# Optimization experiments

Measured on AMD Instinct MI355X. Metric: run time of the kernel, lower is better.

The kernel has to match this reference:

```python
import jax, jax.numpy as jnp
import numpy as np

S, I, H, O = 8192, 1024, 1024, 1024


def setup_inputs() -> dict:
    key = jax.random.key(0)
    ks = jax.random.split(key, 7)
    s = 1.0 / np.sqrt(H).astype(np.float32)  # PyTorch LSTM/Linear init scale
    u = lambda k, shape: jax.random.uniform(k, shape, jnp.float32, -s, s)
    return {
        "x": jax.random.normal(ks[0], (S, I), jnp.float32),
        "W_ih": u(ks[1], (4 * H, I)),   # gate order: i, f, g, o (PyTorch)
        "W_hh": u(ks[2], (4 * H, H)),
        "b_ih": u(ks[3], (4 * H,)),
        "b_hh": u(ks[4], (4 * H,)),
        "W_out": u(ks[5], (O, H)),
        "b_out": u(ks[6], (O,)),
    }


def _lstm_forward(x, W_ih, W_hh, b_ih, b_hh, W_out, b_out):
    h_dim = W_hh.shape[1]
    # Precompute input projections for all timesteps in one GEMM: [S, 4H]
    x_proj = x @ W_ih.T + (b_ih + b_hh)

    def step(carry, xp_t):
        h, c = carry                       # [H], [H]
        gates = xp_t + h @ W_hh.T          # [4H]
        i, f, g, o = jnp.split(gates, 4)
        i = jax.nn.sigmoid(i)
        f = jax.nn.sigmoid(f)
        g = jnp.tanh(g)
        o = jax.nn.sigmoid(o)
        c = f * c + i * g
        h = o * jnp.tanh(c)
        return (h, c), h

    init = (jnp.zeros((h_dim,), x.dtype), jnp.zeros((h_dim,), x.dtype))
    _, hs = jax.lax.scan(step, init, x_proj)   # hs: [S, H]
    logits = hs @ W_out.T + b_out              # [S, O]
    return jax.nn.log_softmax(logits, axis=1)


def reference(x, W_ih, W_hh, b_ih, b_hh, W_out, b_out):
    return _lstm_forward(x, W_ih, W_hh, b_ih, b_hh, W_out, b_out)
```

## Files before the change

kernel.cpp:

```cpp
#include <hip/hip_runtime.h>


using u16 = unsigned short;
using u32 = unsigned int;
using u64 = unsigned long long;

typedef short  short8  __attribute__((ext_vector_type(8)));
typedef float  floatx4 __attribute__((ext_vector_type(4)));
typedef u32    uintx4  __attribute__((ext_vector_type(4)));

#define S_LEN 8192
#define NPROD 64

__device__ __forceinline__ u16 f2bf(float f) {
    u32 u = __float_as_uint(f);
    u += 0x7FFFu + ((u >> 16) & 1u);
    return (u16)(u >> 16);
}

__device__ __forceinline__ floatx4 mfma16(short8 a, short8 b, floatx4 c) {
    return __builtin_amdgcn_mfma_f32_16x16x32_bf16(a, b, c, 0, 0, 0);
}


__global__ void cvt_f32_bf16(const float* __restrict__ src, u16* __restrict__ dst, int n) {
    for (int i = blockIdx.x * blockDim.x + threadIdx.x; i < n; i += gridDim.x * blockDim.x)
        dst[i] = f2bf(src[i]);
}

__global__ void bias_comb_k(const float* __restrict__ a, const float* __restrict__ b,
                            float* __restrict__ o) {
    int i = blockIdx.x * blockDim.x + threadIdx.x;
    if (i < 4096) o[i] = a[i] + b[i];
}

__global__ void init_hbuf(u64* __restrict__ hbuf) {
    hbuf[blockIdx.x * 256 + threadIdx.x] = 0ull;
}


__global__ __launch_bounds__(256) void gemm_bt(const u16* __restrict__ A,
                                               const u16* __restrict__ B,
                                               const float* __restrict__ bias,
                                               float* __restrict__ C,
                                               int M, int N, int K) {
    const int tid = threadIdx.x;
    const int l = tid & 63, w = tid >> 6;
    const int m0 = blockIdx.x * 128 + (w >> 1) * 64;
    const int n0 = blockIdx.y * 64 + (w & 1) * 32;
    const int lr = l & 15, lk = (l >> 4) * 8;

    floatx4 acc[4][2];
#pragma unroll
    for (int i = 0; i < 4; i++)
#pragma unroll
        for (int j = 0; j < 2; j++) acc[i][j] = floatx4{0.f, 0.f, 0.f, 0.f};

    const u16* Ap = A + (size_t)(m0 + lr) * K + lk;
    const u16* Bp = B + (size_t)(n0 + lr) * K + lk;

    for (int k0 = 0; k0 < K; k0 += 32) {
        short8 a0 = *(const short8*)(Ap + k0);
        short8 a1 = *(const short8*)(Ap + (size_t)16 * K + k0);
        short8 a2 = *(const short8*)(Ap + (size_t)32 * K + k0);
        short8 a3 = *(const short8*)(Ap + (size_t)48 * K + k0);
        short8 b0 = *(const short8*)(Bp + k0);
        short8 b1 = *(const short8*)(Bp + (size_t)16 * K + k0);
        acc[0][0] = mfma16(a0, b0, acc[0][0]); acc[0][1] = mfma16(a0, b1, acc[0][1]);
        acc[1][0] = mfma16(a1, b0, acc[1][0]); acc[1][1] = mfma16(a1, b1, acc[1][1]);
        acc[2][0] = mfma16(a2, b0, acc[2][0]); acc[2][1] = mfma16(a2, b1, acc[2][1]);
        acc[3][0] = mfma16(a3, b0, acc[3][0]); acc[3][1] = mfma16(a3, b1, acc[3][1]);
    }

    const int rr = (l >> 4) * 4;
#pragma unroll
    for (int j = 0; j < 2; j++) {
        const int n = n0 + j * 16 + lr;
        const float bv = bias[n];
#pragma unroll
        for (int i = 0; i < 4; i++) {
            const int m = m0 + i * 16 + rr;
#pragma unroll
            for (int r = 0; r < 4; r++)
                C[(size_t)(m + r) * N + n] = acc[i][j][r] + bv;
        }
    }
}


__device__ __forceinline__ float sig_f(float x) {
    return __builtin_amdgcn_rcpf(1.f + __expf(-x));
}
__device__ __forceinline__ float tanh_f(float x) {
    return 1.f - 2.f * __builtin_amdgcn_rcpf(1.f + __expf(2.f * x));
}

__global__ __launch_bounds__(512, 2) void lstm_rec(const u16* __restrict__ Whhb,
                                                   const float* __restrict__ xp,
                                                   u64* __restrict__ hbuf,
                                                   u32* __restrict__ hs) {
    const int p = blockIdx.x;
    const int tid = threadIdx.x;
    const int l = tid & 63, w = tid >> 6;
    const int g = w & 3;
    const int kh = w >> 2;

    __shared__ u32 h_lds[512];
    __shared__ float dots[128];
    __shared__ float xp_lds[2][64];

    short8 afr[16];
    {
        const u16* wr = Whhb + (size_t)(g * 1024 + p * 16 + (l & 15)) * 1024
                       + kh * 512 + ((l >> 4) * 8);
#pragma unroll
        for (int kb = 0; kb < 16; ++kb) afr[kb] = *(const short8*)(wr + kb * 32);
    }
    h_lds[tid] = 0u;

    float c_state = 0.f;
    const float* xprow = xp + (size_t)(l >> 4) * 1024 + p * 16 + (l & 15);
    if (w == 5) xp_lds[0][l] = xprow[0];
    __syncthreads();

    const int bofs = (l >> 4) * 4;
    const u32* hb_base = &h_lds[kh * 256 + bofs];
    const int pi = (w - 1) * 64 + l;

    for (int t = 0; t < S_LEN; ++t) {
        float xc = 0.f;

        if (w == 0) {
            xc = xp_lds[t & 1][l];
        } else if (w == 5) {
            int tn = (t + 1 < S_LEN) ? t + 1 : S_LEN - 1;
            xp_lds[(t + 1) & 1][l] = xprow[(size_t)tn * 4096];
        } else if (w <= 4 && t > 0) {
            u64* src0 = hbuf + (size_t)(t & 1) * 512 + 2 * pi;
            const u32 want = (u32)t;
            uintx4 q;
            bool got = false;
            for (int it = 0; it < 4096 && !got; ++it) {
                asm volatile("global_load_dwordx4 %0, %1, off sc0 sc1\n\t"
                             "s_waitcnt vmcnt(0)"
                             : "=&v"(q) : "v"(src0) : "memory");
                got = (q.y == want) && (q.w == want);
            }
            while (!got) {
                u64 a = __hip_atomic_load(src0, __ATOMIC_RELAXED,
                                          __HIP_MEMORY_SCOPE_AGENT);
                u64 b = __hip_atomic_load(src0 + 1, __ATOMIC_RELAXED,
                                          __HIP_MEMORY_SCOPE_AGENT);
                if ((u32)(a >> 32) == want && (u32)(b >> 32) == want) {
                    q.x = (u32)a; q.z = (u32)b; got = true;
                }
            }
            h_lds[2 * pi]     = q.x;
            h_lds[2 * pi + 1] = q.z;
        }
        __syncthreads();

        floatx4 ac0 = floatx4{0,0,0,0}, ac1 = floatx4{0,0,0,0};
        floatx4 ac2 = floatx4{0,0,0,0}, ac3 = floatx4{0,0,0,0};
#pragma unroll
        for (int kb = 0; kb < 16; kb += 4) {
            uintx4 b0 = *(const uintx4*)(hb_base + (kb + 0) * 16);
            uintx4 b1 = *(const uintx4*)(hb_base + (kb + 1) * 16);
            uintx4 b2 = *(const uintx4*)(hb_base + (kb + 2) * 16);
            uintx4 b3 = *(const uintx4*)(hb_base + (kb + 3) * 16);
            ac0 = mfma16(afr[kb + 0], __builtin_bit_cast(short8, b0), ac0);
            ac1 = mfma16(afr[kb + 1], __builtin_bit_cast(short8, b1), ac1);
            ac2 = mfma16(afr[kb + 2], __builtin_bit_cast(short8, b2), ac2);
            ac3 = mfma16(afr[kb + 3], __builtin_bit_cast(short8, b3), ac3);
        }
        floatx4 acs = (ac0 + ac1) + (ac2 + ac3);
        if ((l & 15) == 0) {
            const int q = l >> 4;
#pragma unroll
            for (int r = 0; r < 4; ++r) dots[kh * 64 + g * 16 + q * 4 + r] = acs[r];
        }
        __syncthreads();

        if (w == 0) {
            float a = dots[l] + dots[64 + l] + xc;
            float act = ((l >> 4) == 2) ? tanh_f(a) : sig_f(a);
            const int jj = l & 15;
            float fi = __shfl(act, jj);
            float ff = __shfl(act, 16 + jj);
            float fg = __shfl(act, 32 + jj);
            float fo = __shfl(act, 48 + jj);
            if (l < 16) {
                c_state = ff * c_state + fi * fg;
                float h = fo * tanh_f(c_state);
                u16 hb16 = f2bf(h);
                u32 other = (u32)__shfl_down((int)hb16, 1);
                if ((l & 1) == 0) {
                    u32 pk = (u32)hb16 | (other << 16);
                    int pidx = p * 8 + (l >> 1);
                    u64 tv = ((u64)(u32)(t + 1) << 32) | (u64)pk;
                    __hip_atomic_store(&hbuf[(size_t)((t + 1) & 1) * 512 + pidx], tv,
                                       __ATOMIC_RELAXED, __HIP_MEMORY_SCOPE_AGENT);
                    hs[(size_t)t * 512 + pidx] = pk;
                }
            }
        }
    }
}


__global__ __launch_bounds__(256) void lsm_k(float* __restrict__ C) {
    const int tid = threadIdx.x;
    float* p = C + (size_t)blockIdx.x * 1024;
    float v0 = p[tid], v1 = p[tid + 256], v2 = p[tid + 512], v3 = p[tid + 768];
    float mx = fmaxf(fmaxf(v0, v1), fmaxf(v2, v3));
#pragma unroll
    for (int o = 1; o < 64; o <<= 1) mx = fmaxf(mx, __shfl_xor(mx, o));
    __shared__ float red[4];
    const int w = tid >> 6, l = tid & 63;
    if (l == 0) red[w] = mx;
    __syncthreads();
    mx = fmaxf(fmaxf(red[0], red[1]), fmaxf(red[2], red[3]));
    float s = __expf(v0 - mx) + __expf(v1 - mx) + __expf(v2 - mx) + __expf(v3 - mx);
#pragma unroll
    for (int o = 1; o < 64; o <<= 1) s += __shfl_xor(s, o);
    __syncthreads();
    if (l == 0) red[w] = s;
    __syncthreads();
    s = red[0] + red[1] + red[2] + red[3];
    float ls = __logf(s) + mx;
    p[tid] = v0 - ls; p[tid + 256] = v1 - ls; p[tid + 512] = v2 - ls; p[tid + 768] = v3 - ls;
}


extern "C" void kernel_launch(void* const* d_in, const int* in_sizes, int n_in,
                              void* d_out, int out_size, void* d_ws, size_t ws_size,
                              hipStream_t stream) {
    const float* x     = (const float*)d_in[0];
    const float* W_ih  = (const float*)d_in[1];
    const float* W_hh  = (const float*)d_in[2];
    const float* b_ih  = (const float*)d_in[3];
    const float* b_hh  = (const float*)d_in[4];
    const float* W_out = (const float*)d_in[5];
    const float* b_out = (const float*)d_in[6];

    char* ws = (char*)d_ws;
    u16*   xb    = (u16*)(ws + 0);
    u16*   Wihb  = (u16*)(ws + 16777216);
    u16*   Whhb  = (u16*)(ws + 25165824);
    u16*   Woutb = (u16*)(ws + 33554432);
    float* biasc = (float*)(ws + 35651584);
    u64*   hbuf  = (u64*)(ws + 35667968);
    u32*   hs    = (u32*)(ws + 35676160);
    float* xp    = (float*)(ws + 52453376);

    init_hbuf<<<4, 256, 0, stream>>>(hbuf);
    cvt_f32_bf16<<<2048, 256, 0, stream>>>(x, xb, 8192 * 1024);
    cvt_f32_bf16<<<1024, 256, 0, stream>>>(W_ih, Wihb, 4096 * 1024);
    cvt_f32_bf16<<<1024, 256, 0, stream>>>(W_hh, Whhb, 4096 * 1024);
    cvt_f32_bf16<<<256, 256, 0, stream>>>(W_out, Woutb, 1024 * 1024);
    bias_comb_k<<<16, 256, 0, stream>>>(b_ih, b_hh, biasc);

    gemm_bt<<<dim3(64, 64), 256, 0, stream>>>(xb, Wihb, biasc, xp, 8192, 4096, 1024);

    lstm_rec<<<NPROD, 512, 0, stream>>>(Whhb, xp, hbuf, hs);

    gemm_bt<<<dim3(64, 16), 256, 0, stream>>>((const u16*)hs, Woutb, b_out, (float*)d_out,
                                              8192, 1024, 1024);

    lsm_k<<<8192, 256, 0, stream>>>((float*)d_out);
}
```

Measured before the change: 13.23 ms.

## Halve recurrent producer blocks, each computing 32 hidden units per step

The persistent LSTM recurrence kernel now uses 32 blocks instead of 64. Each block holds two 16-row slices of W_hh per gate in registers and computes 32 hidden units per timestep. The goal is to cut the number of cross-block flag polls and publishers in the per-step grid-wide handoff, at the cost of twice the MFMA and activation work per block. An unused PROBE macro is also added.

Result: slower. 15.59 ms (+17.8%).

```diff
diff --git a/kernel.cpp b/kernel.cpp
--- a/kernel.cpp
+++ b/kernel.cpp
@@ -10,7 +10,7 @@
 typedef u32    uintx4  __attribute__((ext_vector_type(4)));
 
 #define S_LEN 8192
-#define NPROD 64
+#define NPROD 32
 
 __device__ __forceinline__ u16 f2bf(float f) {
     u32 u = __float_as_uint(f);
@@ -21,6 +21,10 @@
 __device__ __forceinline__ floatx4 mfma16(short8 a, short8 b, floatx4 c) {
     return __builtin_amdgcn_mfma_f32_16x16x32_bf16(a, b, c, 0, 0, 0);
 }
+
+#define PROBE(dst, srcp)                                               \
+    asm volatile("global_load_dwordx4 %0, %1, off sc0 sc1"             \
+                 : "=&v"(dst) : "v"(srcp) : "memory")
 
 
 __global__ void cvt_f32_bf16(const float* __restrict__ src, u16* __restrict__ dst, int n) {
@@ -106,36 +110,41 @@
     const int kh = w >> 2;
 
     __shared__ u32 h_lds[512];
-    __shared__ float dots[128];
-    __shared__ float xp_lds[2][64];
-
-    short8 afr[16];
+    __shared__ float dots2[256];
+    __shared__ float xp_lds[2][128];
+
+    short8 afr0[16], afr1[16];
     {
-        const u16* wr = Whhb + (size_t)(g * 1024 + p * 16 + (l & 15)) * 1024
-                       + kh * 512 + ((l >> 4) * 8);
-#pragma unroll
-        for (int kb = 0; kb < 16; ++kb) afr[kb] = *(const short8*)(wr + kb * 32);
+        const u16* wr0 = Whhb + (size_t)(g * 1024 + p * 32 + (l & 15)) * 1024
+                        + kh * 512 + ((l >> 4) * 8);
+        const u16* wr1 = wr0 + (size_t)16 * 1024;
+#pragma unroll
+        for (int kb = 0; kb < 16; ++kb) {
+            afr0[kb] = *(const short8*)(wr0 + kb * 32);
+            afr1[kb] = *(const short8*)(wr1 + kb * 32);
+        }
     }
     h_lds[tid] = 0u;
-
-    float c_state = 0.f;
-    const float* xprow = xp + (size_t)(l >> 4) * 1024 + p * 16 + (l & 15);
-    if (w == 5) xp_lds[0][l] = xprow[0];
+    if (tid < 256) ((u32*)dots2)[tid] = 0u;
+
+    float c0 = 0.f, c1 = 0.f;
+    const float* xprow = xp + (size_t)(l >> 4) * 1024 + p * 32 + (l & 15);
+    if (w == 5) {
+        xp_lds[0][(l >> 4) * 32 + (l & 15)]      = xprow[0];
+        xp_lds[0][(l >> 4) * 32 + (l & 15) + 16] = xprow[16];
+    }
     __syncthreads();
 
-    const int bofs = (l >> 4) * 4;
-    const u32* hb_base = &h_lds[kh * 256 + bofs];
+    const u32* hb_base = &h_lds[kh * 256 + (l >> 4) * 4];
     const int pi = (w - 1) * 64 + l;
 
     for (int t = 0; t < S_LEN; ++t) {
-        float xc = 0.f;
-
-        if (w == 0) {
-            xc = xp_lds[t & 1][l];
-        } else if (w == 5) {
+        if (w == 5) {
             int tn = (t + 1 < S_LEN) ? t + 1 : S_LEN - 1;
-            xp_lds[(t + 1) & 1][l] = xprow[(size_t)tn * 4096];
-        } else if (w <= 4 && t > 0) {
+            const float* r = xprow + (size_t)tn * 4096;
+            xp_lds[(t + 1) & 1][(l >> 4) * 32 + (l & 15)]      = r[0];
+            xp_lds[(t + 1) & 1][(l >> 4) * 32 + (l & 15) + 16] = r[16];
+        } else if (w >= 1 && w <= 4 && t > 0) {
             u64* src0 = hbuf + (size_t)(t & 1) * 512 + 2 * pi;
             const u32 want = (u32)t;
             uintx4 q;
@@ -160,47 +169,71 @@
         }
         __syncthreads();
 
-        floatx4 ac0 = floatx4{0,0,0,0}, ac1 = floatx4{0,0,0,0};
-        floatx4 ac2 = floatx4{0,0,0,0}, ac3 = floatx4{0,0,0,0};
+        floatx4 a00 = floatx4{0,0,0,0}, a01 = floatx4{0,0,0,0};
+        floatx4 a02 = floatx4{0,0,0,0}, a03 = floatx4{0,0,0,0};
+        floatx4 a10 = floatx4{0,0,0,0}, a11 = floatx4{0,0,0,0};
+        floatx4 a12 = floatx4{0,0,0,0}, a13 = floatx4{0,0,0,0};
 #pragma unroll
         for (int kb = 0; kb < 16; kb += 4) {
             uintx4 b0 = *(const uintx4*)(hb_base + (kb + 0) * 16);
             uintx4 b1 = *(const uintx4*)(hb_base + (kb + 1) * 16);
             uintx4 b2 = *(const uintx4*)(hb_base + (kb + 2) * 16);
             uintx4 b3 = *(const uintx4*)(hb_base + (kb + 3) * 16);
-            ac0 = mfma16(afr[kb + 0], __builtin_bit_cast(short8, b0), ac0);
-            ac1 = mfma16(afr[kb + 1], __builtin_bit_cast(short8, b1), ac1);
-            ac2 = mfma16(afr[kb + 2], __builtin_bit_cast(short8, b2), ac2);
-            ac3 = mfma16(afr[kb + 3], __builtin_bit_cast(short8, b3), ac3);
-        }
-        floatx4 acs = (ac0 + ac1) + (ac2 + ac3);
+            a00 = mfma16(afr0[kb + 0], __builtin_bit_cast(short8, b0), a00);
+            a10 = mfma16(afr1[kb + 0], __builtin_bit_cast(short8, b0), a10);
+            a01 = mfma16(afr0[kb + 1], __builtin_bit_cast(short8, b1), a01);
+            a11 = mfma16(afr1[kb + 1], __builtin_bit_cast(short8, b1), a11);
+            a02 = mfma16(afr0[kb + 2], __builtin_bit_cast(short8, b2), a02);
+            a12 = mfma16(afr1[kb + 2], __builtin_bit_cast(short8, b2), a12);
+            a03 = mfma16(afr0[kb + 3], __builtin_bit_cast(short8, b3), a03);
+            a13 = mfma16(afr1[kb + 3], __builtin_bit_cast(short8, b3), a13);
+        }
+        floatx4 s0 = (a00 + a01) + (a02 + a03);
+        floatx4 s1 = (a10 + a11) + (a12 + a13);
         if ((l & 15) == 0) {
             const int q = l >> 4;
 #pragma unroll
-            for (int r = 0; r < 4; ++r) dots[kh * 64 + g * 16 + q * 4 + r] = acs[r];
+            for (int r = 0; r < 4; ++r) {
+                dots2[kh * 64 + g * 16 + q * 4 + r]       = s0[r];
+                dots2[128 + kh * 64 + g * 16 + q * 4 + r] = s1[r];
+            }
         }
         __syncthreads();
 
         if (w == 0) {
-            float a = dots[l] + dots[64 + l] + xc;
-            float act = ((l >> 4) == 2) ? tanh_f(a) : sig_f(a);
+            float xc0 = xp_lds[t & 1][(l >> 4) * 32 + (l & 15)];
+            float xc1 = xp_lds[t & 1][(l >> 4) * 32 + (l & 15) + 16];
+            float a0 = dots2[l] + dots2[64 + l] + xc0;
+            float a1 = dots2[128 + l] + dots2[192 + l] + xc1;
+            float act0 = ((l >> 4) == 2) ? tanh_f(a0) : sig_f(a0);
+            float act1 = ((l >> 4) == 2) ? tanh_f(a1) : sig_f(a1);
             const int jj = l & 15;
-            float fi = __shfl(act, jj);
-            float ff = __shfl(act, 16 + jj);
-            float fg = __shfl(act, 32 + jj);
-            float fo = __shfl(act, 48 + jj);
+            float fi0 = __shfl(act0, jj),      fi1 = __shfl(act1, jj);
+            float ff0 = __shfl(act0, 16 + jj), ff1 = __shfl(act1, 16 + jj);
+            float fg0 = __shfl(act0, 32 + jj), fg1 = __shfl(act1, 32 + jj);
+            float fo0 = __shfl(act0, 48 + jj), fo1 = __shfl(act1, 48 + jj);
             if (l < 16) {
-                c_state = ff * c_state + fi * fg;
-                float h = fo * tanh_f(c_state);
-                u16 hb16 = f2bf(h);
-                u32 other = (u32)__shfl_down((int)hb16, 1);
+                c0 = ff0 * c0 + fi0 * fg0;
+                c1 = ff1 * c1 + fi1 * fg1;
+                float h0 = fo0 * tanh_f(c0);
+                float h1 = fo1 * tanh_f(c1);
+                u16 hb0 = f2bf(h0), hb1 = f2bf(h1);
+                u32 o0 = (u32)__shfl_down((int)hb0, 1);
+                u32 o1 = (u32)__shfl_down((int)hb1, 1);
                 if ((l & 1) == 0) {
-                    u32 pk = (u32)hb16 | (other << 16);
-                    int pidx = p * 8 + (l >> 1);
-                    u64 tv = ((u64)(u32)(t + 1) << 32) | (u64)pk;
-                    __hip_atomic_store(&hbuf[(size_t)((t + 1) & 1) * 512 + pidx], tv,
+                    u32 pk0 = (u32)hb0 | (o0 << 16);
+                    u32 pk1 = (u32)hb1 | (o1 << 16);
+                    int i0 = p * 16 + (l >> 1);
+                    int i1 = p * 16 + 8 + (l >> 1);
+                    u64 tv0 = ((u64)(u32)(t + 1) << 32) | (u64)pk0;
+                    u64 tv1 = ((u64)(u32)(t + 1) << 32) | (u64)pk1;
+                    const size_t par = (size_t)((t + 1) & 1) * 512;
+                    __hip_atomic_store(&hbuf[par + i0], tv0,
                                        __ATOMIC_RELAXED, __HIP_MEMORY_SCOPE_AGENT);
-                    hs[(size_t)t * 512 + pidx] = pk;
+                    __hip_atomic_store(&hbuf[par + i1], tv1,
+                                       __ATOMIC_RELAXED, __HIP_MEMORY_SCOPE_AGENT);
+                    hs[(size_t)t * 512 + i0] = pk0;
+                    hs[(size_t)t * 512 + i1] = pk1;
                 }
             }
         }
```

## Replace per-step barrier with LDS flags so MFMA starts on partial h

Applied to the files above, without the earlier changes.

The workgroup barrier between the h-fetch and the matvec is replaced by per-wave release/acquire flags in LDS. Each MFMA wave now waits only for the two producer waves that supply its half of the K slice, so it can start on the first half while the second is still arriving. The dots buffer is double-buffered by step parity so the remaining barrier is safe, and wave 0 gets raised priority during the gate math. This adds LDS spin traffic and depends on workgroup-scope atomics ordering being correct.

New measurement: 14.37 ms. 8.6% more time.

```diff
diff --git a/kernel.cpp b/kernel.cpp
--- a/kernel.cpp
+++ b/kernel.cpp
@@ -95,6 +95,10 @@
     return 1.f - 2.f * __builtin_amdgcn_rcpf(1.f + __expf(2.f * x));
 }
 
+#define SPIN_FLAG(idx, tt)                                                      \
+    while (__hip_atomic_load(&hflag[idx], __ATOMIC_ACQUIRE,                     \
+                             __HIP_MEMORY_SCOPE_WORKGROUP) < (u32)(tt)) {}
+
 __global__ __launch_bounds__(512, 2) void lstm_rec(const u16* __restrict__ Whhb,
                                                    const float* __restrict__ xp,
                                                    u64* __restrict__ hbuf,
@@ -106,8 +110,9 @@
     const int kh = w >> 2;
 
     __shared__ u32 h_lds[512];
-    __shared__ float dots[128];
+    __shared__ float dots[2][128];
     __shared__ float xp_lds[2][64];
+    __shared__ u32 hflag[4];
 
     short8 afr[16];
     {
@@ -117,6 +122,7 @@
         for (int kb = 0; kb < 16; ++kb) afr[kb] = *(const short8*)(wr + kb * 32);
     }
     h_lds[tid] = 0u;
+    if (tid < 4) hflag[tid] = 0u;
 
     float c_state = 0.f;
     const float* xprow = xp + (size_t)(l >> 4) * 1024 + p * 16 + (l & 15);
@@ -157,13 +163,16 @@
             }
             h_lds[2 * pi]     = q.x;
             h_lds[2 * pi + 1] = q.z;
-        }
-        __syncthreads();
+            if (l == 0)
+                __hip_atomic_store(&hflag[w - 1], (u32)t, __ATOMIC_RELEASE,
+                                   __HIP_MEMORY_SCOPE_WORKGROUP);
+        }
 
         floatx4 ac0 = floatx4{0,0,0,0}, ac1 = floatx4{0,0,0,0};
         floatx4 ac2 = floatx4{0,0,0,0}, ac3 = floatx4{0,0,0,0};
-#pragma unroll
-        for (int kb = 0; kb < 16; kb += 4) {
+        SPIN_FLAG(2 * kh, t);
+#pragma unroll
+        for (int kb = 0; kb < 8; kb += 4) {
             uintx4 b0 = *(const uintx4*)(hb_base + (kb + 0) * 16);
             uintx4 b1 = *(const uintx4*)(hb_base + (kb + 1) * 16);
             uintx4 b2 = *(const uintx4*)(hb_base + (kb + 2) * 16);
@@ -173,16 +182,30 @@
             ac2 = mfma16(afr[kb + 2], __builtin_bit_cast(short8, b2), ac2);
             ac3 = mfma16(afr[kb + 3], __builtin_bit_cast(short8, b3), ac3);
         }
+        SPIN_FLAG(2 * kh + 1, t);
+#pragma unroll
+        for (int kb = 8; kb < 16; kb += 4) {
+            uintx4 b0 = *(const uintx4*)(hb_base + (kb + 0) * 16);
+            uintx4 b1 = *(const uintx4*)(hb_base + (kb + 1) * 16);
+            uintx4 b2 = *(const uintx4*)(hb_base + (kb + 2) * 16);
+            uintx4 b3 = *(const uintx4*)(hb_base + (kb + 3) * 16);
+            ac0 = mfma16(afr[kb + 0], __builtin_bit_cast(short8, b0), ac0);
+            ac1 = mfma16(afr[kb + 1], __builtin_bit_cast(short8, b1), ac1);
+            ac2 = mfma16(afr[kb + 2], __builtin_bit_cast(short8, b2), ac2);
+            ac3 = mfma16(afr[kb + 3], __builtin_bit_cast(short8, b3), ac3);
+        }
         floatx4 acs = (ac0 + ac1) + (ac2 + ac3);
         if ((l & 15) == 0) {
             const int q = l >> 4;
 #pragma unroll
-            for (int r = 0; r < 4; ++r) dots[kh * 64 + g * 16 + q * 4 + r] = acs[r];
+            for (int r = 0; r < 4; ++r)
+                dots[t & 1][kh * 64 + g * 16 + q * 4 + r] = acs[r];
         }
         __syncthreads();
 
         if (w == 0) {
-            float a = dots[l] + dots[64 + l] + xc;
+            __builtin_amdgcn_s_setprio(1);
+            float a = dots[t & 1][l] + dots[t & 1][64 + l] + xc;
             float act = ((l >> 4) == 2) ? tanh_f(a) : sig_f(a);
             const int jj = l & 15;
             float fi = __shfl(act, jj);
@@ -203,6 +226,7 @@
                     hs[(size_t)t * 512 + pidx] = pk;
                 }
             }
+            __builtin_amdgcn_s_setprio(0);
         }
     }
 }
```
